# Performance work log

Measured on AMD Instinct MI355X. Metric: run time of the kernel, lower is better.

Reference implementation:

```python
import jax, jax.numpy as jnp
import numpy as np

NEG_SLOPE = 0.2
EPS = 1e-16

N = 50000
E = 800000
IN_CH = 128
HID = 64
HEADS = 4
OUT_CH = 128


def setup_inputs() -> dict:
    key = jax.random.key(0)
    ks = jax.random.split(key, 12)
    x = jax.random.normal(ks[0], (N, IN_CH), dtype=jnp.float32)
    edge_index = jax.random.randint(ks[1], (2, E), 0, N, dtype=jnp.int32)
    s1 = 1.0 / np.sqrt(IN_CH)
    s2 = 1.0 / np.sqrt(HID * HEADS)
    # conv1: GATv2Conv(IN_CH -> HID, heads=HEADS, concat=True)
    Wl1 = jax.random.uniform(ks[2], (IN_CH, HEADS * HID), jnp.float32, -s1, s1)
    Wr1 = jax.random.uniform(ks[3], (IN_CH, HEADS * HID), jnp.float32, -s1, s1)
    att1 = jax.random.uniform(ks[4], (HEADS, HID), jnp.float32, -s1, s1)
    b1 = jnp.zeros((HEADS * HID,), jnp.float32)
    # conv2: GATv2Conv(HID*HEADS -> OUT_CH, heads=1, concat=False)
    Wl2 = jax.random.uniform(ks[5], (HEADS * HID, OUT_CH), jnp.float32, -s2, s2)
    Wr2 = jax.random.uniform(ks[6], (HEADS * HID, OUT_CH), jnp.float32, -s2, s2)
    att2 = jax.random.uniform(ks[7], (1, OUT_CH), jnp.float32, -s2, s2)
    b2 = jnp.zeros((OUT_CH,), jnp.float32)
    return {"x": x, "edge_index": edge_index,
            "Wl1": Wl1, "Wr1": Wr1, "att1": att1, "b1": b1,
            "Wl2": Wl2, "Wr2": Wr2, "att2": att2, "b2": b2}


def gatv2_layer(x, src, dst, Wl, Wr, att, bias, heads, ch, concat, num_nodes):
    # x: [N, F_in]; src/dst: [E] (message flows src -> dst)
    xl = (x @ Wl).reshape(num_nodes, heads, ch)  # applied to source nodes
    xr = (x @ Wr).reshape(num_nodes, heads, ch)  # applied to target nodes
    m = xl[src] + xr[dst]                         # [E, H, C]
    e = jnp.sum(jax.nn.leaky_relu(m, NEG_SLOPE) * att[None], axis=-1)  # [E, H]
    # scatter-softmax over incoming edges of each destination node
    emax = jax.ops.segment_max(e, dst, num_segments=num_nodes)  # [N, H]
    ee = jnp.exp(e - emax[dst])
    denom = jax.ops.segment_sum(ee, dst, num_segments=num_nodes)  # [N, H]
    alpha = ee / (denom[dst] + EPS)               # [E, H]
    out = jax.ops.segment_sum(alpha[:, :, None] * xl[src], dst, num_segments=num_nodes)  # [N, H, C]
    if concat:
        out = out.reshape(num_nodes, heads * ch)
    else:
        out = out.mean(axis=1)
    return out + bias


def reference(x, edge_index, Wl1, Wr1, att1, b1, Wl2, Wr2, att2, b2):
    src, dst = edge_index[0], edge_index[1]
    h = gatv2_layer(x, src, dst, Wl1, Wr1, att1, b1, HEADS, HID, True, N)
    h = jax.nn.elu(h)
    # dropout(p=0.3) is identity in eval mode
    out = gatv2_layer(h, src, dst, Wl2, Wr2, att2, b2, 1, OUT_CH, False, N)
    return out
```

## Files before the change

### kernel.cpp

```cpp
#include <hip/hip_runtime.h>
#include <hip/hip_bf16.h>
#include <hip/hip_fp16.h>
#include <math.h>

#define N_NODES 50000
#define E_EDGES 800000
#define NEG_SLOPE 0.2f
#define EPS 1e-16f
#define NB_SCAN ((N_NODES + 255) / 256)

typedef _Float16 f16x8 __attribute__((ext_vector_type(8)));
typedef _Float16 h2f   __attribute__((ext_vector_type(2)));
typedef float    f32x4 __attribute__((ext_vector_type(4)));

__device__ __forceinline__ float leaky(float v) {
    return v > 0.f ? v : NEG_SLOPE * v;
}

__device__ __forceinline__ float dot2acc(h2f a, h2f b, float c) {
#if __has_builtin(__builtin_amdgcn_fdot2)
    return __builtin_amdgcn_fdot2(a, b, c, false);
#else
    return c + (float)a[0] * (float)b[0] + (float)a[1] * (float)b[1];
#endif
}

__device__ __forceinline__ h2f leaky2(h2f s) {
    h2f t = s * (_Float16)NEG_SLOPE;
    return __builtin_elementwise_max(s, t);
}

__device__ __forceinline__ h2f cvt_h2(float x, float y) {
    h2f r; r[0] = (_Float16)x; r[1] = (_Float16)y; return r;
}

__device__ __forceinline__ f16x8 load8(const float* p) {
    const float4 v0 = *(const float4*)p;
    const float4 v1 = *(const float4*)(p + 4);
    f16x8 r;
    r[0] = (_Float16)v0.x; r[1] = (_Float16)v0.y;
    r[2] = (_Float16)v0.z; r[3] = (_Float16)v0.w;
    r[4] = (_Float16)v1.x; r[5] = (_Float16)v1.y;
    r[6] = (_Float16)v1.z; r[7] = (_Float16)v1.w;
    return r;
}
__device__ __forceinline__ f16x8 load8(const _Float16* p) {
    return *(const f16x8*)p;
}

template <typename IT>
__global__ __launch_bounds__(256, 2)
void gemm_mfma(const IT* __restrict__ X, const __half* __restrict__ Wth,
               __half* __restrict__ Y, int Nrows, int K, int M2)
{
    const _Float16* Wt = (const _Float16*)Wth;
    __shared__ _Float16 As[128][40];
    __shared__ _Float16 Bs[256][40];
    const int tid  = threadIdx.x;
    const int row0 = blockIdx.x * 128;
    const int col0 = blockIdx.y * 256;
    const int lane = tid & 63;
    const int wv   = tid >> 6;
    const int wr   = (wv >> 1) * 64;
    const int wc   = (wv & 1) * 128;
    const int fm   = lane & 15;
    const int fk   = (lane >> 4) * 8;
    const int quad = lane >> 4;

    f32x4 acc[4][8] = {};

    for (int k0 = 0; k0 < K; k0 += 32) {
        #pragma unroll
        for (int p = 0; p < 2; ++p) {
            const int idx = tid + p * 256;
            const int r = idx >> 2;
            const int c = (idx & 3) * 8;
            const int gr = row0 + r;
            f16x8 v = {};
            if (gr < Nrows)
                v = load8(X + (size_t)gr * K + k0 + c);
            *(f16x8*)&As[r][c] = v;
        }
        #pragma unroll
        for (int p = 0; p < 4; ++p) {
            const int idx = tid + p * 256;
            const int r = idx >> 2;
            const int c = (idx & 3) * 8;
            *(f16x8*)&Bs[r][c] = *(const f16x8*)(Wt + (size_t)(col0 + r) * K + k0 + c);
        }
        __syncthreads();

        f16x8 bf[8];
        #pragma unroll
        for (int j = 0; j < 8; ++j)
            bf[j] = *(const f16x8*)&Bs[wc + j * 16 + fm][fk];
        #pragma unroll
        for (int i = 0; i < 4; ++i) {
            const f16x8 af = *(const f16x8*)&As[wr + i * 16 + fm][fk];
            #pragma unroll
            for (int j = 0; j < 8; ++j)
                acc[i][j] = __builtin_amdgcn_mfma_f32_16x16x32_f16(af, bf[j], acc[i][j], 0, 0, 0);
        }
        __syncthreads();
    }

    #pragma unroll
    for (int i = 0; i < 4; ++i) {
        #pragma unroll
        for (int j = 0; j < 8; ++j) {
            const int col = col0 + wc + j * 16 + fm;
            #pragma unroll
            for (int rg = 0; rg < 4; ++rg) {
                const int row = row0 + wr + i * 16 + quad * 4 + rg;
                if (row < Nrows)
                    Y[(size_t)row * M2 + col] = __float2half(acc[i][j][rg]);
            }
        }
    }
}

#define CVT_BLOCKS 512
__global__ __launch_bounds__(256)
void cvt_and_hist(const float* __restrict__ Wl1, const float* __restrict__ Wr1,
                  const float* __restrict__ Wl2, const float* __restrict__ Wr2,
                  __half* __restrict__ W1t, __half* __restrict__ W2t,
                  const int* __restrict__ dst, int* __restrict__ deg)
{
    const int b = blockIdx.x;
    if (b < CVT_BLOCKS) {
        int id = b * 256 + threadIdx.x;
        if (id < 512 * 128) {
            const int n = id >> 7, k = id & 127;
            const float* W = (n < 256) ? Wl1 : Wr1;
            const int nn = (n < 256) ? n : n - 256;
            W1t[id] = __float2half(W[(size_t)k * 256 + nn]);
        } else {
            id -= 512 * 128;
            const int n = id >> 8, k = id & 255;
            const float* W = (n < 128) ? Wl2 : Wr2;
            const int nn = (n < 128) ? n : n - 128;
            W2t[id] = __float2half(W[(size_t)k * 128 + nn]);
        }
    } else {
        const int i = (b - CVT_BLOCKS) * 256 + threadIdx.x;
        if (i < E_EDGES) atomicAdd(&deg[dst[i]], 1);
    }
}

__global__ __launch_bounds__(256)
void scan_local(const int* __restrict__ deg, int* __restrict__ locpre,
                int* __restrict__ blockSum)
{
    const int i = blockIdx.x * 256 + threadIdx.x;
    const int lane = threadIdx.x & 63;
    const int wid = threadIdx.x >> 6;
    const int val = (i < N_NODES) ? deg[i] : 0;

    int v = val;
    #pragma unroll
    for (int off = 1; off < 64; off <<= 1) {
        int t = __shfl_up(v, off, 64);
        if (lane >= off) v += t;
    }
    __shared__ int ws[4];
    if (lane == 63) ws[wid] = v;
    __syncthreads();
    int woff = 0;
    for (int k = 0; k < wid; ++k) woff += ws[k];
    if (i < N_NODES) locpre[i] = woff + v - val;
    if (threadIdx.x == 255) blockSum[blockIdx.x] = woff + v;
}

__global__ __launch_bounds__(256)
void scan_final(const int* __restrict__ locpre, const int* __restrict__ blockSum,
                int* __restrict__ rowptr, int* __restrict__ cursor)
{
    const int b = blockIdx.x;
    const int t = threadIdx.x;
    int v = (t < b) ? blockSum[t] : 0;
    #pragma unroll
    for (int off = 32; off; off >>= 1) v += __shfl_xor(v, off, 64);
    __shared__ int ws[4];
    if ((t & 63) == 0) ws[t >> 6] = v;
    __syncthreads();
    const int offset = ws[0] + ws[1] + ws[2] + ws[3];

    const int i = b * 256 + t;
    if (i < N_NODES) {
        const int rp = locpre[i] + offset;
        rowptr[i] = rp;
        cursor[i] = rp;
    }
    if (b == 0 && t == 0) rowptr[N_NODES] = E_EDGES;
}

__global__ __launch_bounds__(256)
void scatter_edges(const int* __restrict__ src, const int* __restrict__ dst,
                   int* __restrict__ cursor, int* __restrict__ ssrc, int E)
{
    int i = blockIdx.x * blockDim.x + threadIdx.x;
    if (i < E) {
        int pos = atomicAdd(&cursor[dst[i]], 1);
        ssrc[pos] = src[i];
    }
}

__global__ __launch_bounds__(256)
void agg1(const __half* __restrict__ xlr, const int* __restrict__ rowptr,
          const int* __restrict__ ssrc, const float* __restrict__ att,
          const float* __restrict__ b, __half* __restrict__ h)
{
    const int w = (blockIdx.x * blockDim.x + threadIdx.x) >> 6;
    if (w >= N_NODES) return;
    const int lane = threadIdx.x & 63;
    const int ch = lane * 4;

    const float4 atf = *(const float4*)(att + ch);
    const h2f at0 = cvt_h2(atf.x, atf.y);
    const h2f at1 = cvt_h2(atf.z, atf.w);
    const float4 bb = *(const float4*)(b + ch);
    union { uint2 u; h2f v[2]; } R;
    R.u = *(const uint2*)(xlr + (size_t)w * 512 + 256 + ch);
    const h2f r0 = R.v[0], r1 = R.v[1];

    float4 a = make_float4(0.f, 0.f, 0.f, 0.f);
    float den = 0.f;

    const int beg = rowptr[w], end = rowptr[w + 1];
    int i = beg;
    while (i + 4 <= end) {
        union { uint2 u; h2f v[2]; } U[4];
        #pragma unroll
        for (int j = 0; j < 4; ++j) {
            const int s = ssrc[i + j];
            U[j].u = *(const uint2*)(xlr + (size_t)s * 512 + ch);
        }
        float m[4];
        #pragma unroll
        for (int j = 0; j < 4; ++j) {
            m[j] = dot2acc(leaky2(U[j].v[0] + r0), at0, 0.f);
            m[j] = dot2acc(leaky2(U[j].v[1] + r1), at1, m[j]);
        }
        #pragma unroll
        for (int off = 1; off < 16; off <<= 1)
            #pragma unroll
            for (int j = 0; j < 4; ++j)
                m[j] += __shfl_xor(m[j], off, 64);
        #pragma unroll
        for (int j = 0; j < 4; ++j) {
            const float e = __expf(m[j]);
            a.x += e * (float)U[j].v[0][0];
            a.y += e * (float)U[j].v[0][1];
            a.z += e * (float)U[j].v[1][0];
            a.w += e * (float)U[j].v[1][1];
            den += e;
        }
        i += 4;
    }
    while (i < end) {
        const int s = ssrc[i];
        union { uint2 u; h2f v[2]; } U;
        U.u = *(const uint2*)(xlr + (size_t)s * 512 + ch);
        float m = dot2acc(leaky2(U.v[0] + r0), at0, 0.f);
        m = dot2acc(leaky2(U.v[1] + r1), at1, m);
        m += __shfl_xor(m, 1, 64);
        m += __shfl_xor(m, 2, 64);
        m += __shfl_xor(m, 4, 64);
        m += __shfl_xor(m, 8, 64);
        const float e = __expf(m);
        a.x += e * (float)U.v[0][0];
        a.y += e * (float)U.v[0][1];
        a.z += e * (float)U.v[1][0];
        a.w += e * (float)U.v[1][1];
        den += e;
        ++i;
    }

    const float inv = 1.f / (den + EPS);
    float v0 = a.x * inv + bb.x;
    float v1 = a.y * inv + bb.y;
    float v2 = a.z * inv + bb.z;
    float v3 = a.w * inv + bb.w;
    v0 = v0 > 0.f ? v0 : __expf(v0) - 1.f;
    v1 = v1 > 0.f ? v1 : __expf(v1) - 1.f;
    v2 = v2 > 0.f ? v2 : __expf(v2) - 1.f;
    v3 = v3 > 0.f ? v3 : __expf(v3) - 1.f;
    union { uint2 u; __half2 h2[2]; } O;
    O.h2[0] = __floats2half2_rn(v0, v1);
    O.h2[1] = __floats2half2_rn(v2, v3);
    *(uint2*)(h + (size_t)w * 256 + ch) = O.u;
}

__global__ __launch_bounds__(256)
void agg2(const __half* __restrict__ xlr, const int* __restrict__ rowptr,
          const int* __restrict__ ssrc, const float* __restrict__ att,
          const float* __restrict__ b, float* __restrict__ out)
{
    const int w = (blockIdx.x * blockDim.x + threadIdx.x) >> 6;
    if (w >= N_NODES) return;
    const int lane = threadIdx.x & 63;
    const int half = lane >> 5;
    const int ch = (lane & 31) * 4;

    const float4 atf = *(const float4*)(att + ch);
    const h2f at0 = cvt_h2(atf.x, atf.y);
    const h2f at1 = cvt_h2(atf.z, atf.w);
    const float4 bb = *(const float4*)(b + ch);
    union { uint2 u; h2f v[2]; } R;
    R.u = *(const uint2*)(xlr + (size_t)w * 256 + 128 + ch);
    const h2f r0 = R.v[0], r1 = R.v[1];

    float4 a = make_float4(0.f, 0.f, 0.f, 0.f);
    float den = 0.f;

    const int beg = rowptr[w], end = rowptr[w + 1];
    int i = beg + half;
    while (i + 2 < end) {
        union { uint2 u; h2f v[2]; } U[2];
        #pragma unroll
        for (int j = 0; j < 2; ++j) {
            const int s = ssrc[i + 2 * j];
            U[j].u = *(const uint2*)(xlr + (size_t)s * 256 + ch);
        }
        float m[2];
        #pragma unroll
        for (int j = 0; j < 2; ++j) {
            m[j] = dot2acc(leaky2(U[j].v[0] + r0), at0, 0.f);
            m[j] = dot2acc(leaky2(U[j].v[1] + r1), at1, m[j]);
        }
        #pragma unroll
        for (int off = 1; off < 32; off <<= 1)
            #pragma unroll
            for (int j = 0; j < 2; ++j)
                m[j] += __shfl_xor(m[j], off, 64);
        #pragma unroll
        for (int j = 0; j < 2; ++j) {
            const float e = __expf(m[j]);
            a.x += e * (float)U[j].v[0][0];
            a.y += e * (float)U[j].v[0][1];
            a.z += e * (float)U[j].v[1][0];
            a.w += e * (float)U[j].v[1][1];
            den += e;
        }
        i += 4;
    }
    if (i < end) {
        const int s = ssrc[i];
        union { uint2 u; h2f v[2]; } U;
        U.u = *(const uint2*)(xlr + (size_t)s * 256 + ch);
        float m = dot2acc(leaky2(U.v[0] + r0), at0, 0.f);
        m = dot2acc(leaky2(U.v[1] + r1), at1, m);
        #pragma unroll
        for (int off = 1; off < 32; off <<= 1)
            m += __shfl_xor(m, off, 64);
        const float e = __expf(m);
        a.x += e * (float)U.v[0][0];
        a.y += e * (float)U.v[0][1];
        a.z += e * (float)U.v[1][0];
        a.w += e * (float)U.v[1][1];
        den += e;
    }

    a.x += __shfl_xor(a.x, 32, 64);
    a.y += __shfl_xor(a.y, 32, 64);
    a.z += __shfl_xor(a.z, 32, 64);
    a.w += __shfl_xor(a.w, 32, 64);
    den += __shfl_xor(den, 32, 64);

    if (half == 0) {
        const float inv = 1.f / (den + EPS);
        float4 o;
        o.x = a.x * inv + bb.x;
        o.y = a.y * inv + bb.y;
        o.z = a.z * inv + bb.z;
        o.w = a.w * inv + bb.w;
        *(float4*)(out + (size_t)w * 128 + ch) = o;
    }
}

extern "C" void kernel_launch(void* const* d_in, const int* in_sizes, int n_in,
                              void* d_out, int out_size, void* d_ws, size_t ws_size,
                              hipStream_t stream)
{
    const float* x    = (const float*)d_in[0];
    const int*   ei   = (const int*)d_in[1];
    const float* Wl1  = (const float*)d_in[2];
    const float* Wr1  = (const float*)d_in[3];
    const float* att1 = (const float*)d_in[4];
    const float* b1   = (const float*)d_in[5];
    const float* Wl2  = (const float*)d_in[6];
    const float* Wr2  = (const float*)d_in[7];
    const float* att2 = (const float*)d_in[8];
    const float* b2   = (const float*)d_in[9];
    const int* src = ei;
    const int* dst = ei + E_EDGES;
    float* out = (float*)d_out;

    __half* xlr1 = (__half*)d_ws;
    __half* hh   = xlr1 + (size_t)N_NODES * 512;
    __half* W1t  = hh + (size_t)N_NODES * 256;
    __half* W2t  = W1t + 512 * 128;
    int* rowptr   = (int*)(W2t + 256 * 256);
    int* cursor   = rowptr + (N_NODES + 1);
    int* deg      = cursor + N_NODES;
    int* ssrc     = deg + N_NODES;
    int* locpre   = ssrc + E_EDGES;
    int* blockSum = locpre + N_NODES;
    __half* xlr2 = xlr1;

    const dim3 blk(256);
    const int gemm_gx = (N_NODES + 127) / 128;
    const int hist_blocks = (E_EDGES + 255) / 256;

    hipMemsetAsync(deg, 0, N_NODES * sizeof(int), stream);
    cvt_and_hist<<<CVT_BLOCKS + hist_blocks, blk, 0, stream>>>(
        Wl1, Wr1, Wl2, Wr2, W1t, W2t, dst, deg);
    scan_local<<<NB_SCAN, blk, 0, stream>>>(deg, locpre, blockSum);
    scan_final<<<NB_SCAN, blk, 0, stream>>>(locpre, blockSum, rowptr, cursor);
    scatter_edges<<<hist_blocks, blk, 0, stream>>>(src, dst, cursor, ssrc, E_EDGES);

    gemm_mfma<float><<<dim3(gemm_gx, 2), blk, 0, stream>>>(x, W1t, xlr1, N_NODES, 128, 512);
    agg1<<<(N_NODES * 64 + 255) / 256, blk, 0, stream>>>(xlr1, rowptr, ssrc, att1, b1, hh);

    gemm_mfma<_Float16><<<dim3(gemm_gx, 1), blk, 0, stream>>>((const _Float16*)hh, W2t, xlr2, N_NODES, 256, 256);
    agg2<<<(N_NODES * 64 + 255) / 256, blk, 0, stream>>>(xlr2, rowptr, ssrc, att2, b2, out);
}
```

Baseline: 336.1 us.

## Use single-pass decoupled-lookback scan and fuse edge scatter into first GEMM

Replaces the two-kernel degree scan with a single-pass scan that takes a block ticket and does decoupled lookback through atomic flag/value pairs. Folds the edge-scatter work into the first GEMM launch as extra leading blocks, so scatter and GEMM run concurrently in one kernel. This removes two kernel launches and the serial gap between scatter and GEMM. In exchange it needs a larger memset for the ticket and state words, and the lookback spins on flags, which depends on earlier-ticketed blocks making forward progress.

```diff
diff --git a/kernel.cpp b/kernel.cpp
--- a/kernel.cpp
+++ b/kernel.cpp
@@ -8,14 +8,12 @@
 #define NEG_SLOPE 0.2f
 #define EPS 1e-16f
 #define NB_SCAN ((N_NODES + 255) / 256)
+#define SC_BLOCKS ((E_EDGES + 255) / 256)
+#define GX1 ((N_NODES + 127) / 128)
 
 typedef _Float16 f16x8 __attribute__((ext_vector_type(8)));
 typedef _Float16 h2f   __attribute__((ext_vector_type(2)));
 typedef float    f32x4 __attribute__((ext_vector_type(4)));
-
-__device__ __forceinline__ float leaky(float v) {
-    return v > 0.f ? v : NEG_SLOPE * v;
-}
 
 __device__ __forceinline__ float dot2acc(h2f a, h2f b, float c) {
 #if __has_builtin(__builtin_amdgcn_fdot2)
@@ -48,17 +46,33 @@
     return *(const f16x8*)p;
 }
 
-template <typename IT>
+template <typename IT, bool FUSE_SCATTER>
 __global__ __launch_bounds__(256, 2)
 void gemm_mfma(const IT* __restrict__ X, const __half* __restrict__ Wth,
-               __half* __restrict__ Y, int Nrows, int K, int M2)
-{
-    const _Float16* Wt = (const _Float16*)Wth;
+               __half* __restrict__ Y, int Nrows, int K, int M2, int gx,
+               const int* __restrict__ src, const int* __restrict__ dst,
+               int* __restrict__ cursor, int* __restrict__ ssrc)
+{
     __shared__ _Float16 As[128][40];
     __shared__ _Float16 Bs[256][40];
+
+    int b = blockIdx.x;
+    if (FUSE_SCATTER) {
+        if (b < SC_BLOCKS) {
+            const int i = b * 256 + threadIdx.x;
+            if (i < E_EDGES) {
+                int pos = atomicAdd(&cursor[dst[i]], 1);
+                ssrc[pos] = src[i];
+            }
+            return;
+        }
+        b -= SC_BLOCKS;
+    }
+
+    const _Float16* Wt = (const _Float16*)Wth;
     const int tid  = threadIdx.x;
-    const int row0 = blockIdx.x * 128;
-    const int col0 = blockIdx.y * 256;
+    const int row0 = (b % gx) * 128;
+    const int col0 = (b / gx) * 256;
     const int lane = tid & 63;
     const int wv   = tid >> 6;
     const int wr   = (wv >> 1) * 64;
@@ -148,10 +162,17 @@
 }
 
 __global__ __launch_bounds__(256)
-void scan_local(const int* __restrict__ deg, int* __restrict__ locpre,
-                int* __restrict__ blockSum)
-{
-    const int i = blockIdx.x * 256 + threadIdx.x;
+void scan_onepass(const int* __restrict__ deg, unsigned long long* __restrict__ state,
+                  int* __restrict__ ticket, int* __restrict__ rowptr,
+                  int* __restrict__ cursor)
+{
+    __shared__ int s_bid;
+    __shared__ int ws[4];
+    __shared__ int s_run;
+    if (threadIdx.x == 0) s_bid = atomicAdd(ticket, 1);
+    __syncthreads();
+    const int bid = s_bid;
+    const int i = bid * 256 + threadIdx.x;
     const int lane = threadIdx.x & 63;
     const int wid = threadIdx.x >> 6;
     const int val = (i < N_NODES) ? deg[i] : 0;
@@ -162,47 +183,39 @@
         int t = __shfl_up(v, off, 64);
         if (lane >= off) v += t;
     }
-    __shared__ int ws[4];
     if (lane == 63) ws[wid] = v;
     __syncthreads();
     int woff = 0;
     for (int k = 0; k < wid; ++k) woff += ws[k];
-    if (i < N_NODES) locpre[i] = woff + v - val;
-    if (threadIdx.x == 255) blockSum[blockIdx.x] = woff + v;
-}
-
-__global__ __launch_bounds__(256)
-void scan_final(const int* __restrict__ locpre, const int* __restrict__ blockSum,
-                int* __restrict__ rowptr, int* __restrict__ cursor)
-{
-    const int b = blockIdx.x;
-    const int t = threadIdx.x;
-    int v = (t < b) ? blockSum[t] : 0;
-    #pragma unroll
-    for (int off = 32; off; off >>= 1) v += __shfl_xor(v, off, 64);
-    __shared__ int ws[4];
-    if ((t & 63) == 0) ws[t >> 6] = v;
+    const int locincl = woff + v;
+    const int total = ws[0] + ws[1] + ws[2] + ws[3];
+
+    if (threadIdx.x == 0) {
+        const unsigned long long fl = (bid == 0) ? 2ULL : 1ULL;
+        __hip_atomic_store(&state[bid], (fl << 32) | (unsigned)total,
+                           __ATOMIC_RELEASE, __HIP_MEMORY_SCOPE_AGENT);
+        int run = 0;
+        if (bid > 0) {
+            int t = bid - 1;
+            while (true) {
+                const unsigned long long st =
+                    __hip_atomic_load(&state[t], __ATOMIC_ACQUIRE, __HIP_MEMORY_SCOPE_AGENT);
+                const unsigned fl2 = (unsigned)(st >> 32);
+                if (fl2 == 2u) { run += (int)(unsigned)st; break; }
+                if (fl2 == 1u) { run += (int)(unsigned)st; --t; }
+            }
+            __hip_atomic_store(&state[bid], (2ULL << 32) | (unsigned)(run + total),
+                               __ATOMIC_RELEASE, __HIP_MEMORY_SCOPE_AGENT);
+        }
+        s_run = run;
+    }
     __syncthreads();
-    const int offset = ws[0] + ws[1] + ws[2] + ws[3];
-
-    const int i = b * 256 + t;
+    const int off = s_run + locincl - val;
     if (i < N_NODES) {
-        const int rp = locpre[i] + offset;
-        rowptr[i] = rp;
-        cursor[i] = rp;
-    }
-    if (b == 0 && t == 0) rowptr[N_NODES] = E_EDGES;
-}
-
-__global__ __launch_bounds__(256)
-void scatter_edges(const int* __restrict__ src, const int* __restrict__ dst,
-                   int* __restrict__ cursor, int* __restrict__ ssrc, int E)
-{
-    int i = blockIdx.x * blockDim.x + threadIdx.x;
-    if (i < E) {
-        int pos = atomicAdd(&cursor[dst[i]], 1);
-        ssrc[pos] = src[i];
-    }
+        rowptr[i] = off;
+        cursor[i] = off;
+    }
+    if (bid == 0 && threadIdx.x == 0) rowptr[N_NODES] = E_EDGES;
 }
 
 __global__ __launch_bounds__(256)
@@ -403,25 +416,26 @@
     int* rowptr   = (int*)(W2t + 256 * 256);
     int* cursor   = rowptr + (N_NODES + 1);
     int* deg      = cursor + N_NODES;
-    int* ssrc     = deg + N_NODES;
-    int* locpre   = ssrc + E_EDGES;
-    int* blockSum = locpre + N_NODES;
+    int* ticket   = deg + N_NODES;
+    unsigned long long* state = (unsigned long long*)(ticket + 1);
+    int* ssrc     = (int*)(state + NB_SCAN);
     __half* xlr2 = xlr1;
 
     const dim3 blk(256);
-    const int gemm_gx = (N_NODES + 127) / 128;
-    const int hist_blocks = (E_EDGES + 255) / 256;
-
-    hipMemsetAsync(deg, 0, N_NODES * sizeof(int), stream);
+    const int hist_blocks = SC_BLOCKS;
+
+    hipMemsetAsync(deg, 0, (size_t)N_NODES * 4 + 4 + (size_t)NB_SCAN * 8, stream);
+
     cvt_and_hist<<<CVT_BLOCKS + hist_blocks, blk, 0, stream>>>(
         Wl1, Wr1, Wl2, Wr2, W1t, W2t, dst, deg);
-    scan_local<<<NB_SCAN, blk, 0, stream>>>(deg, locpre, blockSum);
-    scan_final<<<NB_SCAN, blk, 0, stream>>>(locpre, blockSum, rowptr, cursor);
-    scatter_edges<<<hist_blocks, blk, 0, stream>>>(src, dst, cursor, ssrc, E_EDGES);
-
-    gemm_mfma<float><<<dim3(gemm_gx, 2), blk, 0, stream>>>(x, W1t, xlr1, N_NODES, 128, 512);
+
+    scan_onepass<<<NB_SCAN, blk, 0, stream>>>(deg, state, ticket, rowptr, cursor);
+
+    gemm_mfma<float, true><<<SC_BLOCKS + GX1 * 2, blk, 0, stream>>>(
+        x, W1t, xlr1, N_NODES, 128, 512, GX1, src, dst, cursor, ssrc);
     agg1<<<(N_NODES * 64 + 255) / 256, blk, 0, stream>>>(xlr1, rowptr, ssrc, att1, b1, hh);
 
-    gemm_mfma<_Float16><<<dim3(gemm_gx, 1), blk, 0, stream>>>((const _Float16*)hh, W2t, xlr2, N_NODES, 256, 256);
+    gemm_mfma<_Float16, false><<<GX1, blk, 0, stream>>>(
+        (const _Float16*)hh, W2t, xlr2, N_NODES, 256, 256, GX1, nullptr, nullptr, nullptr, nullptr);
     agg2<<<(N_NODES * 64 + 255) / 256, blk, 0, stream>>>(xlr2, rowptr, ssrc, att2, b2, out);
 }
```

Measured after the change: 367.7 us. 1.09x slower.
